# Performance work log

Hardware: AMD Instinct MI355X
Metric: run time of the kernel (lower is better)

The kernel has to match this reference:

```python
import jax, jax.numpy as jnp
import numpy as np

B, DP, N = 8, 3, 2048
DM, K = 128, 20
C4 = DM // 4


def _gather(pts, idx):
    # pts: (b, n, c), idx: (b, n, k) -> (b, n, k, c)
    return jax.vmap(lambda p, i: p[i])(pts, idx)


def _bn(x, gamma, beta, eps=1e-5):
    # train-mode BatchNorm1d; x: (b, c, n), stats over (batch, points)
    mu = jnp.mean(x, axis=(0, 2), keepdims=True)
    var = jnp.var(x, axis=(0, 2), keepdims=True)
    return gamma[None, :, None] * (x - mu) * jax.lax.rsqrt(var + eps) + beta[None, :, None]


def setup_inputs() -> dict:
    key = jax.random.key(0)
    ks = iter(jax.random.split(key, 32))

    def U(shape):
        s = 1.0 / np.sqrt(shape[-1])
        return jax.random.uniform(next(ks), shape, jnp.float32, -s, s)

    d = {}
    d['features'] = jax.random.normal(next(ks), (B, DP, N), jnp.float32)
    d['fc1_w'] = U((DM, DP)); d['fc1_b'] = U((DM,))
    d['fc2_w'] = U((DM, DM)); d['fc2_b'] = U((DM,))
    d['bn_g'] = jnp.ones((DM,), jnp.float32); d['bn_b'] = jnp.zeros((DM,), jnp.float32)
    d['fb1_w'] = U((DM, 2 * DP)); d['fb1_b'] = U((DM,))
    d['fb2_w'] = U((DM, DM)); d['fb2_b'] = U((DM,))
    d['fg1_w'] = U((DM, DM)); d['fg1_b'] = U((DM,))
    d['fg2_w'] = U((DM, DM)); d['fg2_b'] = U((DM,))
    d['wq'] = U((DM, DM)); d['wk'] = U((DM, DM)); d['wv'] = U((DM, DM))
    d['sa_qk_w'] = U((C4, DM))  # q_conv and k_conv share this weight
    d['sa_v_w'] = U((DM, DM)); d['sa_v_b'] = U((DM,))
    d['sa_t_w'] = U((DM, DM)); d['sa_t_b'] = U((DM,))
    d['sa_bn_g'] = jnp.ones((DM,), jnp.float32); d['sa_bn_b'] = jnp.zeros((DM,), jnp.float32)
    return d


def reference(features, fc1_w, fc1_b, fc2_w, fc2_b, bn_g, bn_b,
              fb1_w, fb1_b, fb2_w, fb2_b, fg1_w, fg1_b, fg2_w, fg2_b,
              wq, wk, wv, sa_qk_w, sa_v_w, sa_v_b, sa_t_w, sa_t_b,
              sa_bn_g, sa_bn_b):
    x = features  # (b, dp, n)
    # --- kNN: negative squared pairwise distance, top-k largest = nearest ---
    inner = -2.0 * jnp.einsum('bdn,bdm->bnm', x, x)
    xx = jnp.sum(x * x, axis=1)  # (b, n)
    pd = -xx[:, :, None] - inner - xx[:, None, :]  # (b, n, n)
    idx = jax.lax.top_k(pd, K)[1]  # (b, n, K) neighbor indices
    # --- get_graph_feature: gather neighbors, concat (nbr - ctr, ctr) ---
    xt = jnp.transpose(x, (0, 2, 1))  # (b, n, dp)
    nbr = _gather(xt, idx)  # (b, n, K, dp)
    ctr = jnp.broadcast_to(xt[:, :, None, :], nbr.shape)
    kf = jnp.concatenate([nbr - ctr, ctr], axis=-1)  # (b, n, K, 2*dp)
    # fb edge MLP
    kf = jax.nn.relu(kf @ fb1_w.T + fb1_b) @ fb2_w.T + fb2_b  # (b, n, K, DM)
    # --- point-transformer attention ---
    x1 = xt @ fc1_w.T + fc1_b  # (b, n, DM)
    q = x1 @ wq.T
    kg = _gather(x1 @ wk.T, idx)  # (b, n, K, DM)
    vg = _gather(x1 @ wv.T, idx)  # (b, n, K, DM)
    a = q[:, :, None, :] - kg + kf
    a = jax.nn.relu(a @ fg1_w.T + fg1_b) @ fg2_w.T + fg2_b  # fc_gamma
    attn = jax.nn.log_softmax(a / jnp.sqrt(jnp.float32(DM)), axis=-2)  # over K
    res = jnp.einsum('bnkf,bnkf->bnf', attn, vg + kf)  # (b, n, DM)
    res = jnp.transpose(res @ fc2_w.T + fc2_b, (0, 2, 1))  # (b, DM, n)
    res = jax.nn.relu(_bn(res, bn_g, bn_b)) + jnp.transpose(x1, (0, 2, 1))
    # --- SA_Layer: offset self-attention (q and k share weights) ---
    xqk = jnp.einsum('cd,bdn->bcn', sa_qk_w, res)  # (b, C4, n)
    energy = jnp.einsum('bcn,bcm->bnm', xqk, xqk)  # (b, n, n)
    att = jax.nn.softmax(energy, axis=-1)
    att = att / (1e-9 + jnp.sum(att, axis=1, keepdims=True))
    xv = jnp.einsum('cd,bdn->bcn', sa_v_w, res) + sa_v_b[None, :, None]
    xr = jnp.einsum('bcn,bnm->bcm', xv, att)  # x_v @ attention
    xr = jnp.einsum('cd,bdn->bcn', sa_t_w, res - xr) + sa_t_b[None, :, None]
    xr = jax.nn.relu(_bn(xr, sa_bn_g, sa_bn_b))
    out = res + xr  # (b, DM, n)
    return (jnp.transpose(out, (0, 2, 1)), attn)
```

## Files before the change

kernel.cpp:

```cpp
#include <hip/hip_runtime.h>

#define NPTS 16384
#define NB 2048
#define KNN 20

typedef __attribute__((ext_vector_type(4))) float f32x4;
typedef __attribute__((ext_vector_type(8))) short short8;

union U4S8 { uint4 q; short8 s; };
union W4   { unsigned u[4]; short8 s; };

__device__ __forceinline__ unsigned bf16_rne(float v){
    unsigned u = __float_as_uint(v);
    return (u + 0x7fffu + ((u>>16)&1u)) >> 16;
}
__device__ __forceinline__ unsigned pack_hl(float v){
    unsigned hi = bf16_rne(v);
    float r = v - __uint_as_float(hi<<16);
    unsigned lo = bf16_rne(r);
    return hi | (lo<<16);
}
__device__ __forceinline__ void split_hl(uint4 w0, uint4 w1, short8& hi, short8& lo){
    W4 h, l;
    h.u[0] = __builtin_amdgcn_perm(w0.y, w0.x, 0x05040100u);
    l.u[0] = __builtin_amdgcn_perm(w0.y, w0.x, 0x07060302u);
    h.u[1] = __builtin_amdgcn_perm(w0.w, w0.z, 0x05040100u);
    l.u[1] = __builtin_amdgcn_perm(w0.w, w0.z, 0x07060302u);
    h.u[2] = __builtin_amdgcn_perm(w1.y, w1.x, 0x05040100u);
    l.u[2] = __builtin_amdgcn_perm(w1.y, w1.x, 0x07060302u);
    h.u[3] = __builtin_amdgcn_perm(w1.w, w1.z, 0x05040100u);
    l.u[3] = __builtin_amdgcn_perm(w1.w, w1.z, 0x07060302u);
    hi = h.s; lo = l.s;
}
__device__ __forceinline__ f32x4 e3_mfma(short8 Ah, short8 Al, short8 Bh, short8 Bl){
    f32x4 acc = (f32x4){0.f,0.f,0.f,0.f};
    acc = __builtin_amdgcn_mfma_f32_16x16x32_bf16(Al, Bh, acc, 0,0,0);
    acc = __builtin_amdgcn_mfma_f32_16x16x32_bf16(Ah, Bl, acc, 0,0,0);
    acc = __builtin_amdgcn_mfma_f32_16x16x32_bf16(Ah, Bh, acc, 0,0,0);
    return acc;
}

__global__ void transpose_kernel(const float* in, float* out, int C){
    int gid = blockIdx.x*256 + threadIdx.x;
    if (gid >= 128*C) return;
    int j = gid / C, c = gid - j*C;
    out[gid] = in[c*128 + j];
}

__global__ void pack_bfrag_kernel(const float* w0, const float* w1, const float* w2, unsigned short* out){
    int gid = blockIdx.x*256 + threadIdx.x;
    if (gid >= 3*16384) return;
    int m = gid >> 14, r = gid & 16383;
    const float* W = (m==0)?w0:(m==1)?w1:w2;
    int e = r & 7, lane = (r>>3) & 63, ks = (r>>9)&3, ct = r>>11;
    int c = ct*16 + (lane&15), j = ks*32 + (lane>>4)*8 + e;
    out[gid] = (unsigned short)bf16_rne(W[c*128 + j]);
}

__global__ __launch_bounds__(256) void knn_kernel(const float* feat, int* g_idx){
    __shared__ float sx[2048], sy[2048], sz[2048];
    __shared__ int swin[32*20];
    int tid = threadIdx.x;
    int p0 = blockIdx.x * 32;
    int b = p0 >> 11;
    const float* fb = feat + b*3*2048;
    for (int i = tid; i < 2048; i += 256){ sx[i]=fb[i]; sy[i]=fb[2048+i]; sz[i]=fb[4096+i]; }
    __syncthreads();

    int chunk = tid & 7, pl = tid >> 3;
    int n = (p0 + pl) & 2047;
    double xi = sx[n], yi = sy[n], zi = sz[n];

    const double SENT = __longlong_as_double(0x7FE0000000000000ll);
    double val[20];
#pragma unroll
    for (int k=0;k<20;k++) val[k] = SENT;

    int base = chunk*256;
    for (int ii=0; ii<256; ii++){
        int i = (ii + (chunk<<2)) & 255;
        int j = base + i;
        double dx = (double)sx[j]-xi, dy = (double)sy[j]-yi, dz = (double)sz[j]-zi;
        double d2 = dx*dx + dy*dy + dz*dz;
        long long kb = ((__double_as_longlong(d2) & ~2047ll) | (long long)j) + (1ll<<61);
        double key = __longlong_as_double(kb);
#pragma unroll
        for (int s=19; s>=1; s--)
            val[s] = fmax(val[s-1], fmin(val[s], key));
        val[0] = fmin(val[0], key);
    }

    for (int kk=0; kk<20; kk++){
        double h = val[0];
        h = fmin(h, __shfl_xor(h, 1));
        h = fmin(h, __shfl_xor(h, 2));
        h = fmin(h, __shfl_xor(h, 4));
        if (val[0] == h){
            swin[pl*20 + kk] = (int)(__double_as_longlong(h) & 2047ll);
#pragma unroll
            for (int s=0;s<19;s++) val[s] = val[s+1];
            val[19] = SENT;
        }
    }
    __syncthreads();
    for (int t = tid; t < 640; t += 256)
        g_idx[p0*20 + t] = swin[t];
}

__global__ void x1_kernel(const float* feat, const float* w, const float* bias, float* x1){
    int gid = blockIdx.x*256 + threadIdx.x;
    int p = gid >> 7, c = gid & 127;
    int b = p >> 11, n = p & 2047;
    const float* fb = feat + b*6144 + n;
    float v = bias[c];
    v += w[c*3+0]*fb[0];
    v += w[c*3+1]*fb[2048];
    v += w[c*3+2]*fb[4096];
    x1[gid] = v;
}

__global__ __launch_bounds__(256) void qkv_kernel(const float* x1, const float* wqT, const float* wkT,
                                                  const float* wvT, float* q, float* k1, float* v1){
    __shared__ float sx[16][128];
    int tid = threadIdx.x;
    int p0 = blockIdx.x * 16;
    for (int t = tid; t < 2048; t += 256) sx[t>>7][t&127] = x1[p0*128 + t];
    __syncthreads();
    int cg = tid & 31, pg = tid >> 5, c0 = cg*4;
    float aq[2][4] = {{0,0,0,0},{0,0,0,0}};
    float ak[2][4] = {{0,0,0,0},{0,0,0,0}};
    float av[2][4] = {{0,0,0,0},{0,0,0,0}};
    for (int j=0;j<128;j++){
        float xa = sx[pg][j], xb = sx[pg+8][j];
        float4 wq4 = *(const float4*)&wqT[j*128 + c0];
        float4 wk4 = *(const float4*)&wkT[j*128 + c0];
        float4 wv4 = *(const float4*)&wvT[j*128 + c0];
        const float* wqp = &wq4.x; const float* wkp = &wk4.x; const float* wvp = &wv4.x;
#pragma unroll
        for (int ci=0; ci<4; ci++){
            aq[0][ci] += wqp[ci]*xa; aq[1][ci] += wqp[ci]*xb;
            ak[0][ci] += wkp[ci]*xa; ak[1][ci] += wkp[ci]*xb;
            av[0][ci] += wvp[ci]*xa; av[1][ci] += wvp[ci]*xb;
        }
    }
#pragma unroll
    for (int pp=0; pp<2; pp++){
        int p = p0 + pg + pp*8;
        *(float4*)&q [p*128 + c0] = make_float4(aq[pp][0],aq[pp][1],aq[pp][2],aq[pp][3]);
        *(float4*)&k1[p*128 + c0] = make_float4(ak[pp][0],ak[pp][1],ak[pp][2],ak[pp][3]);
        *(float4*)&v1[p*128 + c0] = make_float4(av[pp][0],av[pp][1],av[pp][2],av[pp][3]);
    }
}

__device__ __forceinline__ void stage_gemm(const unsigned* buf, const unsigned short* wb,
                                           int lane, int ct0, f32x4 acc[5][2]){
    short8 bf[2][4];
#pragma unroll
    for (int ci=0; ci<2; ci++)
#pragma unroll
    for (int ks=0; ks<4; ks++){
        U4S8 u; u.q = *(const uint4*)(wb + ((ct0+ci)*4 + ks)*512 + lane*8);
        bf[ci][ks] = u.s;
    }
#pragma unroll
    for (int rt=0; rt<5; rt++)
#pragma unroll
    for (int ci=0; ci<2; ci++)
        acc[rt][ci] = (f32x4){0.f,0.f,0.f,0.f};
    int abase = (lane&15)*132 + (lane>>4)*8;
#pragma unroll
    for (int rt=0; rt<5; rt++){
#pragma unroll
        for (int ks=0; ks<4; ks++){
            const unsigned* ap = buf + rt*16*132 + ks*32 + abase;
            uint4 w0 = *(const uint4*)ap;
            uint4 w1 = *(const uint4*)(ap+4);
            short8 hi, lo;
            split_hl(w0, w1, hi, lo);
#pragma unroll
            for (int ci=0; ci<2; ci++){
                acc[rt][ci] = __builtin_amdgcn_mfma_f32_16x16x32_bf16(hi, bf[ci][ks], acc[rt][ci], 0,0,0);
                acc[rt][ci] = __builtin_amdgcn_mfma_f32_16x16x32_bf16(lo, bf[ci][ks], acc[rt][ci], 0,0,0);
            }
        }
    }
}

__global__ __launch_bounds__(256, 3) void attn_kernel(
        const float* feat, const int* g_idx, const float* g_q, const float* g_k1, const float* g_v1,
        const unsigned short* wpk,
        const float* fb1w, const float* fb1b, const float* fb2b, const float* fg1b, const float* fg2b,
        float* g_attn, float* g_res){
    __shared__ __align__(16) unsigned buf[80*132];
    __shared__ float sh_q[512];
    __shared__ float sh_e[80*6];
    __shared__ int   sh_ix[80];
    int tid = threadIdx.x;
    int lane = tid & 63, wave = tid >> 6;
    int gp0 = blockIdx.x * 4;
    int b = gp0 >> 11;
    size_t kvbase = (size_t)b*2048*128;

    sh_q[tid]     = g_q[gp0*128 + tid];
    sh_q[tid+256] = g_q[gp0*128 + tid + 256];
    if (tid < 80){
        int r = tid;
        int nb = g_idx[gp0*20 + r];
        sh_ix[r] = nb;
        int p = (r*205) >> 12;
        int n = (gp0 & 2047) + p;
        const float* fbp = feat + b*6144;
        float cx = fbp[n], cy = fbp[2048+n], cz = fbp[4096+n];
        float nx = fbp[nb], ny = fbp[2048+nb], nz = fbp[4096+nb];
        sh_e[r*6+0] = nx-cx; sh_e[r*6+1] = ny-cy; sh_e[r*6+2] = nz-cz;
        sh_e[r*6+3] = cx;    sh_e[r*6+4] = cy;    sh_e[r*6+5] = cz;
    }
    __syncthreads();

    {
        int c = tid & 127, rh = tid >> 7;
        float w0=fb1w[c*6+0], w1=fb1w[c*6+1], w2=fb1w[c*6+2], w3=fb1w[c*6+3], w4=fb1w[c*6+4], w5=fb1w[c*6+5];
        float bb = fb1b[c];
#pragma unroll
        for (int rr=0; rr<40; rr++){
            int r = rr*2 + rh;
            const float* e = &sh_e[r*6];
            float v = bb + w0*e[0]+w1*e[1]+w2*e[2]+w3*e[3]+w4*e[4]+w5*e[5];
            buf[r*132 + c] = pack_hl(fmaxf(v, 0.f));
        }
    }
    __syncthreads();

    int ct0 = wave*2;
    int colA = ct0*16 + (lane&15);
    int colB = colA + 16;
    int quad = lane >> 4;
    f32x4 acc[5][2];
    float kfr[5][2][4];

    stage_gemm(buf, wpk, lane, ct0, acc);
    {
        float bA = fb2b[colA], bB = fb2b[colB];
#pragma unroll
        for (int rt=0; rt<5; rt++)
#pragma unroll
        for (int ci=0; ci<2; ci++){
            int col = ci ? colB : colA;
            float bias = ci ? bB : bA;
#pragma unroll
            for (int reg=0; reg<4; reg++){
                int row = rt*16 + quad*4 + reg;
                float kf = acc[rt][ci][reg] + bias;
                kfr[rt][ci][reg] = kf;
                int p = (row*205)>>12;
                int nb = sh_ix[row];
                float kg = g_k1[kvbase + (size_t)nb*128 + col];
                float ain = sh_q[p*128 + col] - kg + kf;
                acc[rt][ci][reg] = __uint_as_float(pack_hl(ain));
            }
        }
    }
    __syncthreads();
#pragma unroll
    for (int rt=0; rt<5; rt++)
#pragma unroll
    for (int ci=0; ci<2; ci++)
#pragma unroll
    for (int reg=0; reg<4; reg++){
        int row = rt*16 + quad*4 + reg;
        int col = ci ? colB : colA;
        buf[row*132 + col] = __float_as_uint(acc[rt][ci][reg]);
    }
    __syncthreads();

    stage_gemm(buf, wpk + 16384, lane, ct0, acc);
    {
        float bA = fg1b[colA], bB = fg1b[colB];
#pragma unroll
        for (int rt=0; rt<5; rt++)
#pragma unroll
        for (int ci=0; ci<2; ci++){
            float bias = ci ? bB : bA;
#pragma unroll
            for (int reg=0; reg<4; reg++)
                acc[rt][ci][reg] = __uint_as_float(pack_hl(fmaxf(acc[rt][ci][reg] + bias, 0.f)));
        }
    }
    __syncthreads();
#pragma unroll
    for (int rt=0; rt<5; rt++)
#pragma unroll
    for (int ci=0; ci<2; ci++)
#pragma unroll
    for (int reg=0; reg<4; reg++){
        int row = rt*16 + quad*4 + reg;
        int col = ci ? colB : colA;
        buf[row*132 + col] = __float_as_uint(acc[rt][ci][reg]);
    }
    __syncthreads();

    stage_gemm(buf, wpk + 32768, lane, ct0, acc);
    {
        const float SCALE = 0.08838834764831845f;
        const float NEGF  = -3e38f;
        float bA = fg2b[colA], bB = fg2b[colB];
#pragma unroll
        for (int ci=0; ci<2; ci++){
            int col = ci ? colB : colA;
            float bias = ci ? bB : bA;
            float s[5][4], lm[5];
#pragma unroll
            for (int rt=0; rt<5; rt++){
#pragma unroll
                for (int reg=0; reg<4; reg++)
                    s[rt][reg] = (acc[rt][ci][reg] + bias) * SCALE;
                lm[rt] = fmaxf(fmaxf(s[rt][0], s[rt][1]), fmaxf(s[rt][2], s[rt][3]));
            }
            float m[4];
#pragma unroll
            for (int j=0; j<4; j++){
                float c1 = (j<=quad) ? lm[j]   : NEGF;
                float c2 = (j>=quad) ? lm[j+1] : NEGF;
                m[j] = fmaxf(c1, c2);
                m[j] = fmaxf(m[j], __shfl_xor(m[j], 16));
                m[j] = fmaxf(m[j], __shfl_xor(m[j], 32));
            }
            float mp[5];
            mp[0] = m[0];
            mp[1] = (1<=quad) ? m[1] : m[0];
            mp[2] = (2<=quad) ? m[2] : m[1];
            mp[3] = (3<=quad) ? m[3] : m[2];
            mp[4] = m[3];
            float ls[5];
#pragma unroll
            for (int rt=0; rt<5; rt++){
                float e0 = expf(s[rt][0] - mp[rt]);
                float e1 = expf(s[rt][1] - mp[rt]);
                float e2 = expf(s[rt][2] - mp[rt]);
                float e3 = expf(s[rt][3] - mp[rt]);
                ls[rt] = (e0 + e1) + (e2 + e3);
            }
            float L[4];
#pragma unroll
            for (int j=0; j<4; j++){
                float c1 = (j<=quad) ? ls[j]   : 0.f;
                float c2 = (j>=quad) ? ls[j+1] : 0.f;
                float S = c1 + c2;
                S += __shfl_xor(S, 16);
                S += __shfl_xor(S, 32);
                L[j] = m[j] + logf(S);
            }
            float Lp[5];
            Lp[0] = L[0];
            Lp[1] = (1<=quad) ? L[1] : L[0];
            Lp[2] = (2<=quad) ? L[2] : L[1];
            Lp[3] = (3<=quad) ? L[3] : L[2];
            Lp[4] = L[3];
            float pv[5];
#pragma unroll
            for (int rt=0; rt<5; rt++){
                float pacc = 0.f;
#pragma unroll
                for (int reg=0; reg<4; reg++){
                    int row = rt*16 + quad*4 + reg;
                    float at = s[rt][reg] - Lp[rt];
                    g_attn[(size_t)(gp0*20 + row)*128 + col] = at;
                    int nb = sh_ix[row];
                    float vv = g_v1[kvbase + (size_t)nb*128 + col];
                    pacc += at * (vv + kfr[rt][ci][reg]);
                }
                pv[rt] = pacc;
            }
#pragma unroll
            for (int j=0; j<4; j++){
                float c1 = (j<=quad) ? pv[j]   : 0.f;
                float c2 = (j>=quad) ? pv[j+1] : 0.f;
                float P = c1 + c2;
                P += __shfl_xor(P, 16);
                P += __shfl_xor(P, 32);
                pv[j] = P;
            }
            float rv = (quad==0) ? pv[0] : (quad==1) ? pv[1] : (quad==2) ? pv[2] : pv[3];
            g_res[(size_t)(gp0 + quad)*128 + col] = rv;
        }
    }
}

__global__ __launch_bounds__(256) void lin_kernel(const float* X, const float* WT, const float* bias, float* Y){
    __shared__ float sx[16][128];
    int tid = threadIdx.x;
    int p0 = blockIdx.x * 16;
    for (int t = tid; t < 2048; t += 256) sx[t>>7][t&127] = X[p0*128 + t];
    __syncthreads();
    int cg = tid & 31, pg = tid >> 5, c0 = cg*4;
    float a[2][4] = {{0,0,0,0},{0,0,0,0}};
    for (int j=0;j<128;j++){
        float xa = sx[pg][j], xb = sx[pg+8][j];
        float4 w4 = *(const float4*)&WT[j*128 + c0];
        const float* wp = &w4.x;
#pragma unroll
        for (int ci=0;ci<4;ci++){ a[0][ci] += wp[ci]*xa; a[1][ci] += wp[ci]*xb; }
    }
    float4 bv = *(const float4*)&bias[c0];
    const float* bp = &bv.x;
#pragma unroll
    for (int pp=0;pp<2;pp++){
        int p = p0 + pg + pp*8;
        *(float4*)&Y[p*128+c0] = make_float4(a[pp][0]+bp[0], a[pp][1]+bp[1], a[pp][2]+bp[2], a[pp][3]+bp[3]);
    }
}

__global__ __launch_bounds__(256) void l6_kernel(const float* Xa, const float* Xb, const float* WT,
                                                 const float* bias, float* Y){
    __shared__ float sx[16][128];
    int tid = threadIdx.x;
    int p0 = blockIdx.x * 16;
    for (int t = tid; t < 2048; t += 256) sx[t>>7][t&127] = Xa[p0*128 + t] - Xb[p0*128 + t];
    __syncthreads();
    int cg = tid & 31, pg = tid >> 5, c0 = cg*4;
    float a[2][4] = {{0,0,0,0},{0,0,0,0}};
    for (int j=0;j<128;j++){
        float xa = sx[pg][j], xb = sx[pg+8][j];
        float4 w4 = *(const float4*)&WT[j*128 + c0];
        const float* wp = &w4.x;
#pragma unroll
        for (int ci=0;ci<4;ci++){ a[0][ci] += wp[ci]*xa; a[1][ci] += wp[ci]*xb; }
    }
    float4 bv = *(const float4*)&bias[c0];
    const float* bp = &bv.x;
#pragma unroll
    for (int pp=0;pp<2;pp++){
        int p = p0 + pg + pp*8;
        *(float4*)&Y[p*128+c0] = make_float4(a[pp][0]+bp[0], a[pp][1]+bp[1], a[pp][2]+bp[2], a[pp][3]+bp[3]);
    }
}

__global__ __launch_bounds__(256) void l5_kernel(const float* X, const float* WvT, const float* vb,
                                                 const float* WqkT, unsigned* xvt_pk, unsigned* xqk_pk){
    __shared__ float sx[16][128];
    int tid = threadIdx.x;
    int p0 = blockIdx.x * 16;
    for (int t = tid; t < 2048; t += 256) sx[t>>7][t&127] = X[p0*128 + t];
    __syncthreads();
    int cg = tid & 31, pg = tid >> 5, c0 = cg*4;
    {
        float a[2][4] = {{0,0,0,0},{0,0,0,0}};
        for (int j=0;j<128;j++){
            float xa = sx[pg][j], xb = sx[pg+8][j];
            float4 w4 = *(const float4*)&WvT[j*128 + c0];
            const float* wp = &w4.x;
#pragma unroll
            for (int ci=0;ci<4;ci++){ a[0][ci] += wp[ci]*xa; a[1][ci] += wp[ci]*xb; }
        }
        float4 bv = *(const float4*)&vb[c0];
        const float* bp = &bv.x;
#pragma unroll
        for (int pp=0;pp<2;pp++){
            int p = p0 + pg + pp*8;
            int bb = p >> 11, n = p & 2047;
            unsigned* dst = xvt_pk + ((size_t)(bb*64 + (n>>5)))*4096 + (n&31);
#pragma unroll
            for (int ci=0;ci<4;ci++) dst[(c0+ci)*32] = pack_hl(a[pp][ci] + bp[ci]);
        }
    }
    if (cg < 8){
        int cq = cg*4;
        float a[2][4] = {{0,0,0,0},{0,0,0,0}};
        for (int j=0;j<128;j++){
            float xa = sx[pg][j], xb = sx[pg+8][j];
            float4 w4 = *(const float4*)&WqkT[j*32 + cq];
            const float* wp = &w4.x;
#pragma unroll
            for (int ci=0;ci<4;ci++){ a[0][ci] += wp[ci]*xa; a[1][ci] += wp[ci]*xb; }
        }
#pragma unroll
        for (int pp=0;pp<2;pp++){
            int p = p0 + pg + pp*8;
            uint4 w;
            w.x = pack_hl(a[pp][0]); w.y = pack_hl(a[pp][1]);
            w.z = pack_hl(a[pp][2]); w.w = pack_hl(a[pp][3]);
            *(uint4*)&xqk_pk[p*32 + cq] = w;
        }
    }
}

__global__ void bn_stats_kernel(const float* X, float* sums){
    int tid = threadIdx.x;
    int c = tid & 127, half = tid >> 7;
    int r0 = blockIdx.x*128 + half*64;
    float s = 0.f, sq = 0.f;
    for (int r = r0; r < r0+64; r++){
        float v = X[r*128 + c];
        s += v; sq += v*v;
    }
    atomicAdd(&sums[c], s);
    atomicAdd(&sums[128+c], sq);
}

__global__ void bn1_apply_kernel(const float* res2, const float* x1, const float* sums,
                                 const float* g, const float* beta, float* sres){
    int gid = blockIdx.x*256 + threadIdx.x;
    int c = gid & 127;
    float mu = sums[c] * (1.0f/16384.f);
    float var = sums[128+c] * (1.0f/16384.f) - mu*mu;
    float inv = 1.0f / sqrtf(var + 1e-5f);
    float y = g[c]*(res2[gid]-mu)*inv + beta[c];
    sres[gid] = fmaxf(y, 0.f) + x1[gid];
}

__global__ void final_kernel(const float* sres, const float* xr2, const float* sums,
                             const float* g, const float* beta, float* out0){
    int gid = blockIdx.x*256 + threadIdx.x;
    int c = gid & 127;
    float mu = sums[c] * (1.0f/16384.f);
    float var = sums[128+c] * (1.0f/16384.f) - mu*mu;
    float inv = 1.0f / sqrtf(var + 1e-5f);
    float y = g[c]*(xr2[gid]-mu)*inv + beta[c];
    out0[gid] = sres[gid] + fmaxf(y, 0.f);
}

__global__ __launch_bounds__(256) void sa_stats_kernel(const unsigned* xqk_pk, float* rm, float* irs){
    int tid = threadIdx.x;
    int lane = tid & 63, wave = tid >> 6;
    int b = blockIdx.x >> 5;
    int i0 = (blockIdx.x & 31) * 64 + wave*16;
    const unsigned* qb = xqk_pk + (size_t)b*2048*32;
    int quad = lane >> 4, l15 = lane & 15;
    const unsigned* ap = qb + (i0 + l15)*32 + quad*8;
    uint4 a0 = *(const uint4*)ap, a1 = *(const uint4*)(ap+4);
    short8 Ah, Al; split_hl(a0, a1, Ah, Al);

    float m[4] = {-3e38f,-3e38f,-3e38f,-3e38f};
    for (int jt=0; jt<128; jt++){
        const unsigned* bp = qb + (jt*16 + l15)*32 + quad*8;
        uint4 b0 = *(const uint4*)bp, b1 = *(const uint4*)(bp+4);
        short8 Bh, Bl; split_hl(b0,b1,Bh,Bl);
        f32x4 e = (f32x4){0.f,0.f,0.f,0.f};
        e = __builtin_amdgcn_mfma_f32_16x16x32_bf16(Ah, Bh, e, 0,0,0);
#pragma unroll
        for (int r=0;r<4;r++) m[r] = fmaxf(m[r], e[r]);
    }
#pragma unroll
    for (int mk=1; mk<16; mk<<=1)
#pragma unroll
        for (int r=0;r<4;r++) m[r] = fmaxf(m[r], __shfl_xor(m[r], mk));

    float s[4] = {0.f,0.f,0.f,0.f};
    for (int jt=0; jt<128; jt++){
        const unsigned* bp = qb + (jt*16 + l15)*32 + quad*8;
        uint4 b0 = *(const uint4*)bp, b1 = *(const uint4*)(bp+4);
        short8 Bh, Bl; split_hl(b0,b1,Bh,Bl);
        f32x4 e = e3_mfma(Ah,Al,Bh,Bl);
#pragma unroll
        for (int r=0;r<4;r++) s[r] += expf(e[r]-m[r]);
    }
#pragma unroll
    for (int mk=1; mk<16; mk<<=1)
#pragma unroll
        for (int r=0;r<4;r++) s[r] += __shfl_xor(s[r], mk);
    if (l15 == 0){
#pragma unroll
        for (int r=0;r<4;r++){
            int row = i0 + quad*4 + r;
            rm[b*2048+row]  = m[r];
            irs[b*2048+row] = 1.0f/s[r];
        }
    }
}

#define SXV_STR 36
#define ATT_STR 36
#define NSPLIT 4
__global__ __launch_bounds__(256) void sa_xr_part_kernel(const unsigned* xqk_pk, const unsigned* xvt_pk,
                                                         const float* rm, const float* irs,
                                                         float* part, float* cspart){
    __shared__ __align__(16) unsigned sxv[128*SXV_STR];
    __shared__ __align__(16) unsigned attT[32*ATT_STR];
    __shared__ float scs[2][2][16];
    int tid = threadIdx.x;
    int lane = tid & 63, wave = tid >> 6;
    int quad = lane >> 4, l15 = lane & 15;
    int blk = blockIdx.x;
    int mt = blk & 63;
    int b  = (blk >> 6) & 7;
    int ns = blk >> 9;
    int m0 = mt*32;
    int rt = wave >> 1, ct = wave & 1;
    const unsigned* qb = xqk_pk + (size_t)b*2048*32;

    short8 Bmh, Bml;
    {
        const unsigned* bp = qb + (m0 + ct*16 + l15)*32 + quad*8;
        uint4 b0 = *(const uint4*)bp, b1 = *(const uint4*)(bp+4);
        split_hl(b0,b1,Bmh,Bml);
    }
    f32x4 acc[4];
#pragma unroll
    for (int cc=0;cc<4;cc++) acc[cc] = (f32x4){0.f,0.f,0.f,0.f};
    float cs_acc = 0.f;

    int ch0 = ns*16;
    for (int ci16=0; ci16<16; ci16++){
        int chunk = ch0 + ci16;
        int n0 = chunk*32;
        __syncthreads();
        const unsigned* src = xvt_pk + ((size_t)(b*64 + chunk))*4096;
#pragma unroll
        for (int it=0; it<4; it++){
            int u = tid + it*256;
            int c = u >> 3, part_ = u & 7;
            *(uint4*)&sxv[c*SXV_STR + part_*4] = *(const uint4*)(src + u*4);
        }
        const unsigned* ap = qb + (n0 + rt*16 + l15)*32 + quad*8;
        uint4 a0 = *(const uint4*)ap, a1 = *(const uint4*)(ap+4);
        short8 Ah, Al; split_hl(a0,a1,Ah,Al);
        f32x4 e = e3_mfma(Ah,Al,Bmh,Bml);
#pragma unroll
        for (int r=0;r<4;r++){
            int rowg = b*2048 + n0 + rt*16 + quad*4 + r;
            float att = expf(e[r] - rm[rowg]) * irs[rowg];
            cs_acc += att;
            attT[(ct*16+l15)*ATT_STR + rt*16 + quad*4 + r] = pack_hl(att);
        }
        __syncthreads();
        const unsigned* arp = attT + (ct*16+l15)*ATT_STR + quad*8;
        uint4 aa0 = *(const uint4*)arp, aa1 = *(const uint4*)(arp+4);
        short8 Aph, Apl; split_hl(aa0,aa1,Aph,Apl);
#pragma unroll
        for (int cc=0; cc<4; cc++){
            int c0 = (rt*4 + cc)*16;
            const unsigned* xp = &sxv[(c0 + l15)*SXV_STR + quad*8];
            uint4 x0 = *(const uint4*)xp, x1 = *(const uint4*)(xp+4);
            short8 Xh, Xl; split_hl(x0,x1,Xh,Xl);
            acc[cc] = __builtin_amdgcn_mfma_f32_16x16x32_bf16(Apl, Xh, acc[cc], 0,0,0);
            acc[cc] = __builtin_amdgcn_mfma_f32_16x16x32_bf16(Aph, Xl, acc[cc], 0,0,0);
            acc[cc] = __builtin_amdgcn_mfma_f32_16x16x32_bf16(Aph, Xh, acc[cc], 0,0,0);
        }
    }
    cs_acc += __shfl_xor(cs_acc, 16);
    cs_acc += __shfl_xor(cs_acc, 32);
    if (lane < 16) scs[ct][rt][lane] = cs_acc;
    __syncthreads();
    if (tid < 32)
        cspart[(size_t)(ns*8 + b)*2048 + m0 + tid] = scs[tid>>4][0][tid&15] + scs[tid>>4][1][tid&15];
#pragma unroll
    for (int cc=0; cc<4; cc++){
        int c0 = (rt*4 + cc)*16;
#pragma unroll
        for (int r=0;r<4;r++){
            int mloc = ct*16 + quad*4 + r;
            part[((size_t)(ns*8 + b)*2048 + m0 + mloc)*128 + c0 + l15] = acc[cc][r];
        }
    }
}

__global__ void sa_combine_kernel(const float* part, const float* cspart, float* xr){
    int gid = blockIdx.x*256 + threadIdx.x;
    int bm = gid >> 7;
    float cs = cspart[bm] + cspart[bm+16384] + cspart[bm+2*16384] + cspart[bm+3*16384];
    float v  = part[gid] + part[gid+2097152] + part[gid+2*2097152] + part[gid+3*2097152];
    xr[gid] = v * (1.0f/(1e-9f + cs));
}

extern "C" void kernel_launch(void* const* d_in, const int* in_sizes, int n_in,
                              void* d_out, int out_size, void* d_ws, size_t ws_size,
                              hipStream_t stream){
    (void)in_sizes; (void)n_in; (void)out_size; (void)ws_size;
    const float* feat = (const float*)d_in[0];
    const float* fc1w = (const float*)d_in[1];  const float* fc1b = (const float*)d_in[2];
    const float* fc2w = (const float*)d_in[3];  const float* fc2b = (const float*)d_in[4];
    const float* bng  = (const float*)d_in[5];  const float* bnb  = (const float*)d_in[6];
    const float* fb1w = (const float*)d_in[7];  const float* fb1b = (const float*)d_in[8];
    const float* fb2w = (const float*)d_in[9];  const float* fb2b = (const float*)d_in[10];
    const float* fg1w = (const float*)d_in[11]; const float* fg1b = (const float*)d_in[12];
    const float* fg2w = (const float*)d_in[13]; const float* fg2b = (const float*)d_in[14];
    const float* wq   = (const float*)d_in[15]; const float* wk   = (const float*)d_in[16];
    const float* wv   = (const float*)d_in[17];
    const float* saqk = (const float*)d_in[18];
    const float* savw = (const float*)d_in[19]; const float* savb = (const float*)d_in[20];
    const float* satw = (const float*)d_in[21]; const float* satb = (const float*)d_in[22];
    const float* sabng= (const float*)d_in[23]; const float* sabnb= (const float*)d_in[24];

    float* out0 = (float*)d_out;
    float* out1 = out0 + 2097152;

    char* ws = (char*)d_ws;
    size_t off = 0;
    auto A = [&](size_t bytes)->char*{
        char* r = ws + off;
        off = (off + bytes + 255) & ~(size_t)255;
        return r;
    };
    const size_t PBUF = (size_t)NPTS*128*4;
    int*      g_idx  = (int*)A((size_t)NPTS*KNN*4);
    float*    g_x1   = (float*)A(PBUF);
    float*    g_q    = (float*)A(PBUF);
    float*    g_k1   = (float*)A(PBUF);
    float*    g_v1   = (float*)A(PBUF);
    float*    g_res  = (float*)A(PBUF);
    float*    g_res2 = (float*)A(PBUF);
    float*    g_sres = (float*)A(PBUF);
    float*    g_xr   = (float*)A(PBUF);
    float*    g_xr2  = (float*)A(PBUF);
    unsigned* g_xvt_pk = (unsigned*)A((size_t)NPTS*128*4);
    unsigned* g_xqk_pk = (unsigned*)A((size_t)NPTS*32*4);
    float*    g_rm   = (float*)A((size_t)NPTS*4);
    float*    g_rs   = (float*)A((size_t)NPTS*4);
    float*    g_stats= (float*)A((size_t)512*4);
    unsigned short* g_wpk = (unsigned short*)A((size_t)3*16384*2);
    float*    g_wqT  = (float*)A(65536);
    float*    g_wkT  = (float*)A(65536);
    float*    g_wvT  = (float*)A(65536);
    float*    g_fc2T = (float*)A(65536);
    float*    g_savT = (float*)A(65536);
    float*    g_satT = (float*)A(65536);
    float*    g_sqkT = (float*)A(16384);

    float* bn1s = g_stats;
    float* bn2s = g_stats + 256;

    float* g_part   = g_q;
    float* g_cspart = g_res2;

    hipMemsetAsync(g_stats, 0, (size_t)512*4, stream);

    pack_bfrag_kernel<<<192, 256, 0, stream>>>(fb2w, fg1w, fg2w, g_wpk);
    transpose_kernel<<<64, 256, 0, stream>>>(wq,   g_wqT, 128);
    transpose_kernel<<<64, 256, 0, stream>>>(wk,   g_wkT, 128);
    transpose_kernel<<<64, 256, 0, stream>>>(wv,   g_wvT, 128);
    transpose_kernel<<<64, 256, 0, stream>>>(fc2w, g_fc2T, 128);
    transpose_kernel<<<64, 256, 0, stream>>>(savw, g_savT, 128);
    transpose_kernel<<<64, 256, 0, stream>>>(satw, g_satT, 128);
    transpose_kernel<<<16, 256, 0, stream>>>(saqk, g_sqkT, 32);

    knn_kernel<<<512, 256, 0, stream>>>(feat, g_idx);
    x1_kernel<<<8192, 256, 0, stream>>>(feat, fc1w, fc1b, g_x1);
    qkv_kernel<<<1024, 256, 0, stream>>>(g_x1, g_wqT, g_wkT, g_wvT, g_q, g_k1, g_v1);
    attn_kernel<<<4096, 256, 0, stream>>>(feat, g_idx, g_q, g_k1, g_v1, g_wpk,
                                          fb1w, fb1b, fb2b, fg1b, fg2b, out1, g_res);
    lin_kernel<<<1024, 256, 0, stream>>>(g_res, g_fc2T, fc2b, g_res2);
    bn_stats_kernel<<<128, 256, 0, stream>>>(g_res2, bn1s);
    bn1_apply_kernel<<<8192, 256, 0, stream>>>(g_res2, g_x1, bn1s, bng, bnb, g_sres);
    l5_kernel<<<1024, 256, 0, stream>>>(g_sres, g_savT, savb, g_sqkT, g_xvt_pk, g_xqk_pk);
    sa_stats_kernel<<<256, 256, 0, stream>>>(g_xqk_pk, g_rm, g_rs);
    sa_xr_part_kernel<<<512*NSPLIT, 256, 0, stream>>>(g_xqk_pk, g_xvt_pk, g_rm, g_rs, g_part, g_cspart);
    sa_combine_kernel<<<8192, 256, 0, stream>>>(g_part, g_cspart, g_xr);
    l6_kernel<<<1024, 256, 0, stream>>>(g_sres, g_xr, g_satT, satb, g_xr2);
    bn_stats_kernel<<<128, 256, 0, stream>>>(g_xr2, bn2s);
    final_kernel<<<8192, 256, 0, stream>>>(g_sres, g_xr2, bn2s, sabng, sabnb, out0);
}
```

Before: 782.2 us.

## Split LDS staging into separate bf16 hi/lo planes and remap block order per batch

```diff
diff --git a/kernel.cpp b/kernel.cpp
--- a/kernel.cpp
+++ b/kernel.cpp
@@ -14,11 +14,22 @@
     unsigned u = __float_as_uint(v);
     return (u + 0x7fffu + ((u>>16)&1u)) >> 16;
 }
+__device__ __forceinline__ unsigned cvt_pk_bf16(float a, float b){
+    unsigned r;
+    asm("v_cvt_pk_bf16_f32 %0, %1, %2" : "=v"(r) : "v"(a), "v"(b));
+    return r;
+}
 __device__ __forceinline__ unsigned pack_hl(float v){
-    unsigned hi = bf16_rne(v);
-    float r = v - __uint_as_float(hi<<16);
-    unsigned lo = bf16_rne(r);
-    return hi | (lo<<16);
+    unsigned h = cvt_pk_bf16(v, v);
+    float r = v - __uint_as_float(h << 16);
+    unsigned l = cvt_pk_bf16(r, r);
+    return __builtin_amdgcn_perm(l, h, 0x05040100u);
+}
+__device__ __forceinline__ void pack2(float v0, float v1, unsigned& h2, unsigned& l2){
+    h2 = cvt_pk_bf16(v0, v1);
+    float r0 = v0 - __uint_as_float(h2 << 16);
+    float r1 = v1 - __uint_as_float(h2 & 0xffff0000u);
+    l2 = cvt_pk_bf16(r0, r1);
 }
 __device__ __forceinline__ void split_hl(uint4 w0, uint4 w1, short8& hi, short8& lo){
     W4 h, l;
@@ -152,8 +163,9 @@
     }
 }
 
-__device__ __forceinline__ void stage_gemm(const unsigned* buf, const unsigned short* wb,
-                                           int lane, int ct0, f32x4 acc[5][2]){
+#define ASTR 136
+__device__ __forceinline__ void stage_gemm(const unsigned short* bH, const unsigned short* bL,
+                                           const unsigned short* wb, int lane, int ct0, f32x4 acc[5][2]){
     short8 bf[2][4];
 #pragma unroll
     for (int ci=0; ci<2; ci++)
@@ -167,16 +179,14 @@
 #pragma unroll
     for (int ci=0; ci<2; ci++)
         acc[rt][ci] = (f32x4){0.f,0.f,0.f,0.f};
-    int abase = (lane&15)*132 + (lane>>4)*8;
+    int abase = (lane&15)*ASTR + (lane>>4)*8;
 #pragma unroll
     for (int rt=0; rt<5; rt++){
 #pragma unroll
         for (int ks=0; ks<4; ks++){
-            const unsigned* ap = buf + rt*16*132 + ks*32 + abase;
-            uint4 w0 = *(const uint4*)ap;
-            uint4 w1 = *(const uint4*)(ap+4);
-            short8 hi, lo;
-            split_hl(w0, w1, hi, lo);
+            int off = rt*16*ASTR + ks*32 + abase;
+            short8 hi = *(const short8*)(bH + off);
+            short8 lo = *(const short8*)(bL + off);
 #pragma unroll
             for (int ci=0; ci<2; ci++){
                 acc[rt][ci] = __builtin_amdgcn_mfma_f32_16x16x32_bf16(hi, bf[ci][ks], acc[rt][ci], 0,0,0);
@@ -184,6 +194,14 @@
             }
         }
     }
+}
+
+__device__ __forceinline__ void store4(unsigned short* bH, unsigned short* bL,
+                                       int r0, int col, unsigned h2, unsigned l2, unsigned h3, unsigned l3){
+    bH[(r0+0)*ASTR + col] = (unsigned short)h2;        bL[(r0+0)*ASTR + col] = (unsigned short)l2;
+    bH[(r0+1)*ASTR + col] = (unsigned short)(h2>>16);  bL[(r0+1)*ASTR + col] = (unsigned short)(l2>>16);
+    bH[(r0+2)*ASTR + col] = (unsigned short)h3;        bL[(r0+2)*ASTR + col] = (unsigned short)l3;
+    bH[(r0+3)*ASTR + col] = (unsigned short)(h3>>16);  bL[(r0+3)*ASTR + col] = (unsigned short)(l3>>16);
 }
 
 __global__ __launch_bounds__(256, 3) void attn_kernel(
@@ -191,13 +209,16 @@
         const unsigned short* wpk,
         const float* fb1w, const float* fb1b, const float* fb2b, const float* fg1b, const float* fg2b,
         float* g_attn, float* g_res){
-    __shared__ __align__(16) unsigned buf[80*132];
+    __shared__ __align__(16) unsigned short bufH[80*ASTR];
+    __shared__ __align__(16) unsigned short bufL[80*ASTR];
     __shared__ float sh_q[512];
     __shared__ float sh_e[80*6];
     __shared__ int   sh_ix[80];
     int tid = threadIdx.x;
     int lane = tid & 63, wave = tid >> 6;
-    int gp0 = blockIdx.x * 4;
+    int bidx = blockIdx.x;
+    int blk = ((bidx & 7) << 9) | (bidx >> 3);
+    int gp0 = blk * 4;
     int b = gp0 >> 11;
     size_t kvbase = (size_t)b*2048*128;
 
@@ -222,11 +243,15 @@
         float w0=fb1w[c*6+0], w1=fb1w[c*6+1], w2=fb1w[c*6+2], w3=fb1w[c*6+3], w4=fb1w[c*6+4], w5=fb1w[c*6+5];
         float bb = fb1b[c];
 #pragma unroll
-        for (int rr=0; rr<40; rr++){
-            int r = rr*2 + rh;
-            const float* e = &sh_e[r*6];
-            float v = bb + w0*e[0]+w1*e[1]+w2*e[2]+w3*e[3]+w4*e[4]+w5*e[5];
-            buf[r*132 + c] = pack_hl(fmaxf(v, 0.f));
+        for (int t=0; t<20; t++){
+            int r0 = t*4 + rh, r1 = r0 + 2;
+            const float* e0 = &sh_e[r0*6];
+            const float* e1 = &sh_e[r1*6];
+            float v0 = fmaxf(bb + w0*e0[0]+w1*e0[1]+w2*e0[2]+w3*e0[3]+w4*e0[4]+w5*e0[5], 0.f);
+            float v1 = fmaxf(bb + w0*e1[0]+w1*e1[1]+w2*e1[2]+w3*e1[3]+w4*e1[4]+w5*e1[5], 0.f);
+            unsigned h2, l2; pack2(v0, v1, h2, l2);
+            bufH[r0*ASTR + c] = (unsigned short)h2;       bufL[r0*ASTR + c] = (unsigned short)l2;
+            bufH[r1*ASTR + c] = (unsigned short)(h2>>16); bufL[r1*ASTR + c] = (unsigned short)(l2>>16);
         }
     }
     __syncthreads();
@@ -238,7 +263,7 @@
     f32x4 acc[5][2];
     float kfr[5][2][4];
 
-    stage_gemm(buf, wpk, lane, ct0, acc);
+    stage_gemm(bufH, bufL, wpk, lane, ct0, acc);
     {
         float bA = fb2b[colA], bB = fb2b[colB];
 #pragma unroll
@@ -247,6 +272,7 @@
         for (int ci=0; ci<2; ci++){
             int col = ci ? colB : colA;
             float bias = ci ? bB : bA;
+            float ain[4];
 #pragma unroll
             for (int reg=0; reg<4; reg++){
                 int row = rt*16 + quad*4 + reg;
@@ -255,9 +281,13 @@
                 int p = (row*205)>>12;
                 int nb = sh_ix[row];
                 float kg = g_k1[kvbase + (size_t)nb*128 + col];
-                float ain = sh_q[p*128 + col] - kg + kf;
-                acc[rt][ci][reg] = __uint_as_float(pack_hl(ain));
+                ain[reg] = sh_q[p*128 + col] - kg + kf;
             }
+            unsigned h2,l2,h3,l3;
+            pack2(ain[0], ain[1], h2, l2);
+            pack2(ain[2], ain[3], h3, l3);
+            acc[rt][ci][0] = __uint_as_float(h2); acc[rt][ci][1] = __uint_as_float(l2);
+            acc[rt][ci][2] = __uint_as_float(h3); acc[rt][ci][3] = __uint_as_float(l3);
         }
     }
     __syncthreads();
@@ -265,15 +295,12 @@
     for (int rt=0; rt<5; rt++)
 #pragma unroll
     for (int ci=0; ci<2; ci++)
-#pragma unroll
-    for (int reg=0; reg<4; reg++){
-        int row = rt*16 + quad*4 + reg;
-        int col = ci ? colB : colA;
-        buf[row*132 + col] = __float_as_uint(acc[rt][ci][reg]);
-    }
-    __syncthreads();
-
-    stage_gemm(buf, wpk + 16384, lane, ct0, acc);
+        store4(bufH, bufL, rt*16 + quad*4, ci ? colB : colA,
+               __float_as_uint(acc[rt][ci][0]), __float_as_uint(acc[rt][ci][1]),
+               __float_as_uint(acc[rt][ci][2]), __float_as_uint(acc[rt][ci][3]));
+    __syncthreads();
+
+    stage_gemm(bufH, bufL, wpk + 16384, lane, ct0, acc);
     {
         float bA = fg1b[colA], bB = fg1b[colB];
 #pragma unroll
@@ -281,9 +308,15 @@
 #pragma unroll
         for (int ci=0; ci<2; ci++){
             float bias = ci ? bB : bA;
-#pragma unroll
-            for (int reg=0; reg<4; reg++)
-                acc[rt][ci][reg] = __uint_as_float(pack_hl(fmaxf(acc[rt][ci][reg] + bias, 0.f)));
+            float v0 = fmaxf(acc[rt][ci][0] + bias, 0.f);
+            float v1 = fmaxf(acc[rt][ci][1] + bias, 0.f);
+            float v2 = fmaxf(acc[rt][ci][2] + bias, 0.f);
+            float v3 = fmaxf(acc[rt][ci][3] + bias, 0.f);
+            unsigned h2,l2,h3,l3;
+            pack2(v0, v1, h2, l2);
+            pack2(v2, v3, h3, l3);
+            acc[rt][ci][0] = __uint_as_float(h2); acc[rt][ci][1] = __uint_as_float(l2);
+            acc[rt][ci][2] = __uint_as_float(h3); acc[rt][ci][3] = __uint_as_float(l3);
         }
     }
     __syncthreads();
@@ -291,15 +324,12 @@
     for (int rt=0; rt<5; rt++)
 #pragma unroll
     for (int ci=0; ci<2; ci++)
-#pragma unroll
-    for (int reg=0; reg<4; reg++){
-        int row = rt*16 + quad*4 + reg;
-        int col = ci ? colB : colA;
-        buf[row*132 + col] = __float_as_uint(acc[rt][ci][reg]);
-    }
-    __syncthreads();
-
-    stage_gemm(buf, wpk + 32768, lane, ct0, acc);
+        store4(bufH, bufL, rt*16 + quad*4, ci ? colB : colA,
+               __float_as_uint(acc[rt][ci][0]), __float_as_uint(acc[rt][ci][1]),
+               __float_as_uint(acc[rt][ci][2]), __float_as_uint(acc[rt][ci][3]));
+    __syncthreads();
+
+    stage_gemm(bufH, bufL, wpk + 32768, lane, ct0, acc);
     {
         const float SCALE = 0.08838834764831845f;
         const float NEGF  = -3e38f;
@@ -308,13 +338,13 @@
         for (int ci=0; ci<2; ci++){
             int col = ci ? colB : colA;
             float bias = ci ? bB : bA;
-            float s[5][4], lm[5];
+            float lm[5];
 #pragma unroll
             for (int rt=0; rt<5; rt++){
 #pragma unroll
                 for (int reg=0; reg<4; reg++)
-                    s[rt][reg] = (acc[rt][ci][reg] + bias) * SCALE;
-                lm[rt] = fmaxf(fmaxf(s[rt][0], s[rt][1]), fmaxf(s[rt][2], s[rt][3]));
+                    acc[rt][ci][reg] = (acc[rt][ci][reg] + bias) * SCALE;
+                lm[rt] = fmaxf(fmaxf(acc[rt][ci][0], acc[rt][ci][1]), fmaxf(acc[rt][ci][2], acc[rt][ci][3]));
             }
             float m[4];
 #pragma unroll
@@ -334,10 +364,10 @@
             float ls[5];
 #pragma unroll
             for (int rt=0; rt<5; rt++){
-                float e0 = expf(s[rt][0] - mp[rt]);
-                float e1 = expf(s[rt][1] - mp[rt]);
-                float e2 = expf(s[rt][2] - mp[rt]);
-                float e3 = expf(s[rt][3] - mp[rt]);
+                float e0 = expf(acc[rt][ci][0] - mp[rt]);
+                float e1 = expf(acc[rt][ci][1] - mp[rt]);
+                float e2 = expf(acc[rt][ci][2] - mp[rt]);
+                float e3 = expf(acc[rt][ci][3] - mp[rt]);
                 ls[rt] = (e0 + e1) + (e2 + e3);
             }
             float L[4];
@@ -363,7 +393,7 @@
 #pragma unroll
                 for (int reg=0; reg<4; reg++){
                     int row = rt*16 + quad*4 + reg;
-                    float at = s[rt][reg] - Lp[rt];
+                    float at = acc[rt][ci][reg] - Lp[rt];
                     g_attn[(size_t)(gp0*20 + row)*128 + col] = at;
                     int nb = sh_ix[row];
                     float vv = g_v1[kvbase + (size_t)nb*128 + col];
@@ -522,8 +552,8 @@
 __global__ __launch_bounds__(256) void sa_stats_kernel(const unsigned* xqk_pk, float* rm, float* irs){
     int tid = threadIdx.x;
     int lane = tid & 63, wave = tid >> 6;
-    int b = blockIdx.x >> 5;
-    int i0 = (blockIdx.x & 31) * 64 + wave*16;
+    int b = blockIdx.x & 7;
+    int i0 = (blockIdx.x >> 3) * 64 + wave*16;
     const unsigned* qb = xqk_pk + (size_t)b*2048*32;
     int quad = lane >> 4, l15 = lane & 15;
     const unsigned* ap = qb + (i0 + l15)*32 + quad*8;
@@ -580,10 +610,11 @@
     int tid = threadIdx.x;
     int lane = tid & 63, wave = tid >> 6;
     int quad = lane >> 4, l15 = lane & 15;
-    int blk = blockIdx.x;
-    int mt = blk & 63;
-    int b  = (blk >> 6) & 7;
-    int ns = blk >> 9;
+    int bid = blockIdx.x;
+    int b   = bid & 7;
+    int rest = bid >> 3;
+    int ns  = rest >> 6;
+    int mt  = rest & 63;
     int m0 = mt*32;
     int rt = wave >> 1, ct = wave & 1;
     const unsigned* qb = xqk_pk + (size_t)b*2048*32;
```

New measurement: 773.2 us. About the same (-1.1%).
